# Kernel tuning notes

Hardware: AMD Instinct MI355X
Metric: run time of the kernel (lower is better)

## Reference

```python
import jax, jax.numpy as jnp
import numpy as np

S, B, E, H, V, O = 1024, 256, 128, 256, 32000, 2


def setup_inputs() -> dict:
    key = jax.random.key(0)
    ks = jax.random.split(key, 6)
    inp = jax.random.randint(ks[0], (S, B), 0, V)                     # [S, B] time-major token ids
    lengths = jax.random.randint(ks[1], (B,), 1, S + 1)               # valid lengths in [1, S]
    emb_table = jax.random.normal(ks[2], (V, E), jnp.float32) * 0.1   # nn.Embedding weight
    w_ih = jax.random.normal(ks[3], (4 * H, E), jnp.float32) * 0.05   # LSTM weight_ih_l0 (gate order i,f,g,o)
    w_hh = jax.random.normal(ks[4], (4 * H, H), jnp.float32) * 0.05   # LSTM weight_hh_l0
    b_ih = jnp.zeros((4 * H,), jnp.float32)
    b_hh = jnp.zeros((4 * H,), jnp.float32)
    dec_w = jax.random.normal(ks[5], (O, H), jnp.float32) * 0.05      # decoder Linear (bias=False)
    h0 = jnp.zeros((1, B, H), jnp.float32)
    c0 = jnp.zeros((1, B, H), jnp.float32)
    return dict(inp=inp, lengths=lengths, h0=h0, c0=c0, emb_table=emb_table,
                w_ih=w_ih, w_hh=w_hh, b_ih=b_ih, b_hh=b_hh, dec_w=dec_w)


def reference(inp, lengths, h0, c0, emb_table, w_ih, w_hh, b_ih, b_hh, dec_w):
    emb = emb_table[inp]  # [S, B, E]
    bias = b_ih + b_hh

    def step(carry, x_t):
        h, c = carry
        gates = x_t @ w_ih.T + h @ w_hh.T + bias          # [B, 4H]
        i, f, g, o = jnp.split(gates, 4, axis=-1)         # pytorch gate order i,f,g,o
        i, f, o = jax.nn.sigmoid(i), jax.nn.sigmoid(f), jax.nn.sigmoid(o)
        g = jnp.tanh(g)
        c = f * c + i * g
        h = o * jnp.tanh(c)
        return (h, c), (h, c)

    _, (hs, cs) = jax.lax.scan(step, (h0[0], c0[0]), emb)  # hs, cs: [S, B, H]
    idx = lengths - 1
    b_arange = jnp.arange(B)
    last_h = hs[idx, b_arange]                             # [B, H] output at last valid step
    last_c = cs[idx, b_arange]
    decoded = jax.nn.sigmoid(last_h @ dec_w.T)             # [B, O]
    # packed-RNN final hidden = state at each sequence's own last valid step
    return decoded, (last_h[None], last_c[None])
```

## Files before the change

kernel.cpp:

```cpp
#include <hip/hip_runtime.h>
#include <hip/hip_bf16.h>
#include <hip/hip_fp16.h>

#define S_LEN 1024
#define BATCH 256
#define EDIM  128
#define HDIM  256
#define ODIM  2

typedef unsigned int uint32;
typedef unsigned long long uint64;
typedef _Float16 half_t;
typedef half_t half2v __attribute__((ext_vector_type(2)));
typedef half_t half8  __attribute__((ext_vector_type(8)));
typedef float  f32x4  __attribute__((ext_vector_type(4)));

#define OFF_WHHF   0
#define OFF_WIHF   131072
#define OFF_HBUF   196608
#define HBUF_DW    131072

__device__ __forceinline__ float sigf(float x)     { return 1.0f / (1.0f + __expf(-x)); }
__device__ __forceinline__ float tanhfast(float x) { return 1.0f - 2.0f / (__expf(2.0f * x) + 1.0f); }

__device__ __forceinline__ uint32 packh2(float a, float b) {
  union { uint32 u; half2v h; } c; c.h[0] = (half_t)a; c.h[1] = (half_t)b; return c.u;
}
__device__ __forceinline__ half8 as_h8(uint4 v) {
  union { uint4 u; half8 h; } c; c.u = v; return c.h;
}

__global__ void prep_kernel(const float* __restrict__ w_ih, const float* __restrict__ w_hh,
                            uint32* __restrict__ ws_u) {
  int id = blockIdx.x * 256 + threadIdx.x;
  if (id < 131072) {
    int q = id >> 15, T = (id >> 11) & 15, t = (id >> 8) & 7, l = (id >> 2) & 63, d = id & 3;
    int grow = (T >> 2) * 256 + q * 64 + (T & 3) * 16 + (l & 15);
    int k = t * 32 + (l >> 4) * 8 + 2 * d;
    ws_u[OFF_WHHF + id] = packh2(w_hh[grow * HDIM + k], w_hh[grow * HDIM + k + 1]);
  } else if (id < 131072 + 65536) {
    int i2 = id - 131072;
    int q = i2 >> 14, T = (i2 >> 10) & 15, t = (i2 >> 8) & 3, l = (i2 >> 2) & 63, d = i2 & 3;
    int grow = (T >> 2) * 256 + q * 64 + (T & 3) * 16 + (l & 15);
    int k = t * 32 + (l >> 4) * 8 + 2 * d;
    ws_u[OFF_WIHF + i2] = packh2(w_ih[grow * EDIM + k], w_ih[grow * EDIM + k + 1]);
  } else if (id < 131072 + 65536 + HBUF_DW) {
    ws_u[OFF_HBUF + (id - 131072 - 65536)] = 0;
  }
}

__global__ __launch_bounds__(256, 1) void lstm_kernel(
    const int* __restrict__ inp, const int* __restrict__ lengths,
    const float* __restrict__ h0, const float* __restrict__ c0,
    const float* __restrict__ emb,
    const float* __restrict__ b_ih, const float* __restrict__ b_hh,
    uint32* __restrict__ ws_u,
    float* __restrict__ outh, float* __restrict__ outc) {
  __shared__ uint32 x_l[2 * 16 * 68];
  __shared__ uint32 h_l[16 * 132];
  __shared__ int fast_sh;

  const int tid  = threadIdx.x;
  const int lane = tid & 63, w = tid >> 6;
  const int c = blockIdx.x & 15, q = blockIdx.x >> 4;
  const int n = lane & 15, p = lane >> 4;
  const int sb = tid >> 4, j = tid & 15;

  uint64* hb = (uint64*)(ws_u + OFF_HBUF);

  {
    uint32 xcc;
    asm volatile("s_getreg_b32 %0, hwreg(HW_REG_XCC_ID)" : "=s"(xcc));
    if (tid == 0) {
      int* sl = (int*)(ws_u + OFF_HBUF);
      const int sbase = (16 + c) * 4096;
      __hip_atomic_store(sl + sbase + 64 * q, (int)xcc + 1,
                         __ATOMIC_RELAXED, __HIP_MEMORY_SCOPE_AGENT);
      int ok = 1;
      for (int qq = 0; qq < 4; ++qq) {
        if (qq == q) continue;
        int v;
        do {
          v = __hip_atomic_load(sl + sbase + 64 * qq,
                                __ATOMIC_RELAXED, __HIP_MEMORY_SCOPE_AGENT);
        } while (v == 0);
        ok &= (v == (int)xcc + 1);
      }
      fast_sh = ok;
    }
  }

  int perm[8];
  perm[0] = 2 * q; perm[1] = 2 * q + 1;
#pragma unroll
  for (int i = 2; i < 8; ++i) {
    int base = i - 2;
    perm[i] = base < 2 * q ? base : base + 2;
  }
  int haddr[8];
#pragma unroll
  for (int i = 0; i < 8; ++i) haddr[i] = n * 132 + perm[i] * 16 + p * 4;

  uint4 ahh[4][8], aih[4][4];
  {
    const uint4* whhf = (const uint4*)(ws_u + OFF_WHHF);
    const uint4* wihf = (const uint4*)(ws_u + OFF_WIHF);
#pragma unroll
    for (int g = 0; g < 4; ++g) {
      const int T = g * 4 + w;
#pragma unroll
      for (int i = 0; i < 8; ++i)
        ahh[g][i] = whhf[((q * 16 + T) * 8 + perm[i]) * 64 + lane];
#pragma unroll
      for (int t = 0; t < 4; ++t)
        aih[g][t] = wihf[((q * 16 + T) * 4 + t) * 64 + lane];
    }
  }

  const int ub  = 16 * w + 4 * p;
  const int col = 16 * c + n;
  const int len = lengths[col] - 1;
  float bias_[4][4], cst[4];
#pragma unroll
  for (int g = 0; g < 4; ++g) {
    float4 bi = *(const float4*)(b_ih + g * 256 + q * 64 + ub);
    float4 bh = *(const float4*)(b_hh + g * 256 + q * 64 + ub);
    bias_[g][0] = bi.x + bh.x; bias_[g][1] = bi.y + bh.y;
    bias_[g][2] = bi.z + bh.z; bias_[g][3] = bi.w + bh.w;
  }
  {
    float4 cv = *(const float4*)(c0 + col * HDIM + q * 64 + ub);
    cst[0] = cv.x; cst[1] = cv.y; cst[2] = cv.z; cst[3] = cv.w;
  }

  {
    const float4* hsrc = (const float4*)(h0 + (16 * c + sb) * HDIM) + 4 * j;
    float4 a0 = hsrc[0], a1 = hsrc[1], a2 = hsrc[2], a3 = hsrc[3];
    uint4 pk0 = { packh2(a0.x,a0.y), packh2(a0.z,a0.w), packh2(a1.x,a1.y), packh2(a1.z,a1.w) };
    uint4 pk1 = { packh2(a2.x,a2.y), packh2(a2.z,a2.w), packh2(a3.x,a3.y), packh2(a3.z,a3.w) };
    *(uint4*)(h_l + sb * 132 + 8 * j)     = pk0;
    *(uint4*)(h_l + sb * 132 + 8 * j + 4) = pk1;
    int tok = inp[16 * c + sb];
    const float4* xsrc = (const float4*)(emb + tok * EDIM) + 2 * j;
    float4 v0 = xsrc[0], v1 = xsrc[1];
    uint4 px = { packh2(v0.x,v0.y), packh2(v0.z,v0.w), packh2(v1.x,v1.y), packh2(v1.z,v1.w) };
    *(uint4*)(x_l + sb * 68 + 4 * j) = px;
  }
  __syncthreads();
  const bool fast = (fast_sh != 0);

  int ch[6];
#pragma unroll
  for (int i = 0; i < 6; ++i) {
    int idx6 = j * 6 + i;
    ch[i] = idx6 < q * 32 ? idx6 : idx6 + 32;
  }

  for (int s = 0; s < S_LEN; ++s) {
    const int par = s & 1;

    uint64 hv6[6] = {0, 0, 0, 0, 0, 0};
    const uint64* rp = hb + (((par ^ 1) * 16 + c) * 16 + sb) * 128;
    const uint64 *r0 = rp + ch[0], *r1 = rp + ch[1], *r2 = rp + ch[2],
                 *r3 = rp + ch[3], *r4 = rp + ch[4], *r5 = rp + ch[5];
    if (s > 0) {
      hv6[0] = __hip_atomic_load(r0, __ATOMIC_RELAXED, __HIP_MEMORY_SCOPE_AGENT);
      hv6[1] = __hip_atomic_load(r1, __ATOMIC_RELAXED, __HIP_MEMORY_SCOPE_AGENT);
      hv6[2] = __hip_atomic_load(r2, __ATOMIC_RELAXED, __HIP_MEMORY_SCOPE_AGENT);
      hv6[3] = __hip_atomic_load(r3, __ATOMIC_RELAXED, __HIP_MEMORY_SCOPE_AGENT);
      hv6[4] = __hip_atomic_load(r4, __ATOMIC_RELAXED, __HIP_MEMORY_SCOPE_AGENT);
      hv6[5] = __hip_atomic_load(r5, __ATOMIC_RELAXED, __HIP_MEMORY_SCOPE_AGENT);
    }

    f32x4 acc[4];
#pragma unroll
    for (int g = 0; g < 4; ++g)
      acc[g] = (f32x4){ bias_[g][0], bias_[g][1], bias_[g][2], bias_[g][3] };
#pragma unroll
    for (int t = 0; t < 4; ++t) {
      uint4 xb = *(const uint4*)(x_l + par * 1088 + n * 68 + t * 16 + p * 4);
#pragma unroll
      for (int g = 0; g < 4; ++g)
        acc[g] = __builtin_amdgcn_mfma_f32_16x16x32_f16(as_h8(aih[g][t]), as_h8(xb), acc[g], 0, 0, 0);
    }
#pragma unroll
    for (int i = 0; i < 2; ++i) {
      uint4 hbv = *(const uint4*)(h_l + haddr[i]);
#pragma unroll
      for (int g = 0; g < 4; ++g)
        acc[g] = __builtin_amdgcn_mfma_f32_16x16x32_f16(as_h8(ahh[g][i]), as_h8(hbv), acc[g], 0, 0, 0);
    }

    if (s > 0) {
      const uint32 us = (uint32)s;
      while (!(((uint32)(hv6[0] >> 32) >= us) & ((uint32)(hv6[1] >> 32) >= us) &
               ((uint32)(hv6[2] >> 32) >= us) & ((uint32)(hv6[3] >> 32) >= us) &
               ((uint32)(hv6[4] >> 32) >= us) & ((uint32)(hv6[5] >> 32) >= us))) {
        hv6[0] = __hip_atomic_load(r0, __ATOMIC_RELAXED, __HIP_MEMORY_SCOPE_AGENT);
        hv6[1] = __hip_atomic_load(r1, __ATOMIC_RELAXED, __HIP_MEMORY_SCOPE_AGENT);
        hv6[2] = __hip_atomic_load(r2, __ATOMIC_RELAXED, __HIP_MEMORY_SCOPE_AGENT);
        hv6[3] = __hip_atomic_load(r3, __ATOMIC_RELAXED, __HIP_MEMORY_SCOPE_AGENT);
        hv6[4] = __hip_atomic_load(r4, __ATOMIC_RELAXED, __HIP_MEMORY_SCOPE_AGENT);
        hv6[5] = __hip_atomic_load(r5, __ATOMIC_RELAXED, __HIP_MEMORY_SCOPE_AGENT);
      }
#pragma unroll
      for (int i = 0; i < 6; ++i) h_l[sb * 132 + ch[i]] = (uint32)hv6[i];
    }
    __syncthreads();

    float4 xv0 = {0.f,0.f,0.f,0.f}, xv1 = {0.f,0.f,0.f,0.f};
    if (s + 1 < S_LEN) {
      int tok = inp[(s + 1) * BATCH + 16 * c + sb];
      const float4* xsrc = (const float4*)(emb + tok * EDIM) + 2 * j;
      xv0 = xsrc[0]; xv1 = xsrc[1];
    }

#pragma unroll
    for (int i = 2; i < 8; ++i) {
      uint4 hbv = *(const uint4*)(h_l + haddr[i]);
#pragma unroll
      for (int g = 0; g < 4; ++g)
        acc[g] = __builtin_amdgcn_mfma_f32_16x16x32_f16(as_h8(ahh[g][i]), as_h8(hbv), acc[g], 0, 0, 0);
    }

    float hv4[4];
#pragma unroll
    for (int r = 0; r < 4; ++r) {
      float iv = sigf(acc[0][r]), fv = sigf(acc[1][r]);
      float gv = tanhfast(acc[2][r]), ov = sigf(acc[3][r]);
      float cn = fv * cst[r] + iv * gv;
      cst[r] = cn;
      hv4[r] = ov * tanhfast(cn);
    }

    if (s + 1 < S_LEN) {
      uint32 pay0 = packh2(hv4[0], hv4[1]), pay1 = packh2(hv4[2], hv4[3]);
      const uint32 su = (uint32)(s + 1);
      const int P = q * 32 + 8 * w + 2 * p;
      uint64* wp = hb + (((par * 16 + c) * 16 + n) * 128 + P);
      uint64 pv0 = (uint64)pay0 | (((uint64)su) << 32);
      uint64 pv1 = (uint64)pay1 | (((uint64)su) << 32);
      if (fast) {
        __hip_atomic_store(wp,     pv0, __ATOMIC_RELAXED, __HIP_MEMORY_SCOPE_WORKGROUP);
        __hip_atomic_store(wp + 1, pv1, __ATOMIC_RELAXED, __HIP_MEMORY_SCOPE_WORKGROUP);
      } else {
        __hip_atomic_store(wp,     pv0, __ATOMIC_RELAXED, __HIP_MEMORY_SCOPE_AGENT);
        __hip_atomic_store(wp + 1, pv1, __ATOMIC_RELAXED, __HIP_MEMORY_SCOPE_AGENT);
      }
      *(uint2*)(h_l + n * 132 + P) = (uint2){ pay0, pay1 };
      uint4 px = { packh2(xv0.x,xv0.y), packh2(xv0.z,xv0.w), packh2(xv1.x,xv1.y), packh2(xv1.z,xv1.w) };
      *(uint4*)(x_l + (par ^ 1) * 1088 + sb * 68 + 4 * j) = px;
    }
    if (s == len) {
      float4 ho = { hv4[0], hv4[1], hv4[2], hv4[3] };
      float4 co = { cst[0], cst[1], cst[2], cst[3] };
      *(float4*)(outh + col * HDIM + q * 64 + ub) = ho;
      *(float4*)(outc + col * HDIM + q * 64 + ub) = co;
    }
    __syncthreads();
  }
}

__global__ __launch_bounds__(64) void decode_kernel(const float* __restrict__ outh,
                                                    const float* __restrict__ dec_w,
                                                    float* __restrict__ dec) {
  int b = blockIdx.x, l = threadIdx.x;
  float p0 = 0.f, p1 = 0.f;
#pragma unroll
  for (int m = 0; m < HDIM / 64; ++m) {
    float h = outh[b * HDIM + l + 64 * m];
    p0 = fmaf(h, dec_w[l + 64 * m], p0);
    p1 = fmaf(h, dec_w[HDIM + l + 64 * m], p1);
  }
#pragma unroll
  for (int off = 32; off > 0; off >>= 1) {
    p0 += __shfl_down(p0, off);
    p1 += __shfl_down(p1, off);
  }
  if (l == 0) {
    dec[b * ODIM + 0] = sigf(p0);
    dec[b * ODIM + 1] = sigf(p1);
  }
}

extern "C" void kernel_launch(void* const* d_in, const int* in_sizes, int n_in,
                              void* d_out, int out_size, void* d_ws, size_t ws_size,
                              hipStream_t stream) {
  const int*   inp     = (const int*)d_in[0];
  const int*   lengths = (const int*)d_in[1];
  const float* h0      = (const float*)d_in[2];
  const float* c0      = (const float*)d_in[3];
  const float* emb     = (const float*)d_in[4];
  const float* w_ih    = (const float*)d_in[5];
  const float* w_hh    = (const float*)d_in[6];
  const float* b_ih    = (const float*)d_in[7];
  const float* b_hh    = (const float*)d_in[8];
  const float* dec_w   = (const float*)d_in[9];

  uint32* ws_u = (uint32*)d_ws;

  float* dec  = (float*)d_out;
  float* outh = dec + BATCH * ODIM;
  float* outc = outh + BATCH * HDIM;

  const int prep_total = 131072 + 65536 + HBUF_DW;
  prep_kernel<<<(prep_total + 255) / 256, 256, 0, stream>>>(w_ih, w_hh, ws_u);
  lstm_kernel<<<64, 256, 0, stream>>>(inp, lengths, h0, c0, emb, b_ih, b_hh,
                                      ws_u, outh, outc);
  decode_kernel<<<BATCH, 64, 0, stream>>>(outh, dec_w, dec);
}
```

Before: 2.414 ms.

## Feed remote hidden-state loads directly into MFMA registers, drop mid-step barrier

Each lane now polls exactly the remote h fragments it needs for its own MFMA B operand (permuted chunk offsets) and builds the operand in registers, instead of cooperatively copying into LDS and syncing. This removes one __syncthreads per timestep and the LDS round trip, and prefetches the next token id early. The step barrier is replaced by a manual lgkmcnt wait plus s_barrier with sched barriers. It risks more global polling traffic (24 atomic loads per lane instead of 6) and relies on the perm mapping being correct.

```diff
diff --git a/kernel.cpp b/kernel.cpp
--- a/kernel.cpp
+++ b/kernel.cpp
@@ -149,115 +149,127 @@
   __syncthreads();
   const bool fast = (fast_sh != 0);
 
-  int ch[6];
-#pragma unroll
-  for (int i = 0; i < 6; ++i) {
-    int idx6 = j * 6 + i;
-    ch[i] = idx6 < q * 32 ? idx6 : idx6 + 32;
-  }
-
-  for (int s = 0; s < S_LEN; ++s) {
-    const int par = s & 1;
-
-    uint64 hv6[6] = {0, 0, 0, 0, 0, 0};
-    const uint64* rp = hb + (((par ^ 1) * 16 + c) * 16 + sb) * 128;
-    const uint64 *r0 = rp + ch[0], *r1 = rp + ch[1], *r2 = rp + ch[2],
-                 *r3 = rp + ch[3], *r4 = rp + ch[4], *r5 = rp + ch[5];
-    if (s > 0) {
-      hv6[0] = __hip_atomic_load(r0, __ATOMIC_RELAXED, __HIP_MEMORY_SCOPE_AGENT);
-      hv6[1] = __hip_atomic_load(r1, __ATOMIC_RELAXED, __HIP_MEMORY_SCOPE_AGENT);
-      hv6[2] = __hip_atomic_load(r2, __ATOMIC_RELAXED, __HIP_MEMORY_SCOPE_AGENT);
-      hv6[3] = __hip_atomic_load(r3, __ATOMIC_RELAXED, __HIP_MEMORY_SCOPE_AGENT);
-      hv6[4] = __hip_atomic_load(r4, __ATOMIC_RELAXED, __HIP_MEMORY_SCOPE_AGENT);
-      hv6[5] = __hip_atomic_load(r5, __ATOMIC_RELAXED, __HIP_MEMORY_SCOPE_AGENT);
-    }
-
+  const int p4 = p * 4;
+  const int pbA = perm[2] * 16 + p4, pbB = perm[3] * 16 + p4, pbC = perm[4] * 16 + p4;
+  const int pbD = perm[5] * 16 + p4, pbE = perm[6] * 16 + p4, pbF = perm[7] * 16 + p4;
+
+#define AL(ptr) __hip_atomic_load((ptr), __ATOMIC_RELAXED, __HIP_MEMORY_SCOPE_AGENT)
+#define XMF(t) { uint4 xb = *(const uint4*)(x_l + par * 1088 + n * 68 + (t) * 16 + p4); \
+    acc[0] = __builtin_amdgcn_mfma_f32_16x16x32_f16(as_h8(aih[0][t]), as_h8(xb), acc[0], 0, 0, 0); \
+    acc[1] = __builtin_amdgcn_mfma_f32_16x16x32_f16(as_h8(aih[1][t]), as_h8(xb), acc[1], 0, 0, 0); \
+    acc[2] = __builtin_amdgcn_mfma_f32_16x16x32_f16(as_h8(aih[2][t]), as_h8(xb), acc[2], 0, 0, 0); \
+    acc[3] = __builtin_amdgcn_mfma_f32_16x16x32_f16(as_h8(aih[3][t]), as_h8(xb), acc[3], 0, 0, 0); }
+#define HMF(i) { uint4 hbv = *(const uint4*)(h_l + haddr[i]); \
+    acc[0] = __builtin_amdgcn_mfma_f32_16x16x32_f16(as_h8(ahh[0][i]), as_h8(hbv), acc[0], 0, 0, 0); \
+    acc[1] = __builtin_amdgcn_mfma_f32_16x16x32_f16(as_h8(ahh[1][i]), as_h8(hbv), acc[1], 0, 0, 0); \
+    acc[2] = __builtin_amdgcn_mfma_f32_16x16x32_f16(as_h8(ahh[2][i]), as_h8(hbv), acc[2], 0, 0, 0); \
+    acc[3] = __builtin_amdgcn_mfma_f32_16x16x32_f16(as_h8(ahh[3][i]), as_h8(hbv), acc[3], 0, 0, 0); }
+#define HMFR(L, i) { uint4 hbv = { (uint32)h##L##0, (uint32)h##L##1, (uint32)h##L##2, (uint32)h##L##3 }; \
+    acc[0] = __builtin_amdgcn_mfma_f32_16x16x32_f16(as_h8(ahh[0][i]), as_h8(hbv), acc[0], 0, 0, 0); \
+    acc[1] = __builtin_amdgcn_mfma_f32_16x16x32_f16(as_h8(ahh[1][i]), as_h8(hbv), acc[1], 0, 0, 0); \
+    acc[2] = __builtin_amdgcn_mfma_f32_16x16x32_f16(as_h8(ahh[2][i]), as_h8(hbv), acc[2], 0, 0, 0); \
+    acc[3] = __builtin_amdgcn_mfma_f32_16x16x32_f16(as_h8(ahh[3][i]), as_h8(hbv), acc[3], 0, 0, 0); }
+#define GATES_PUBLISH(sv)                                                                 \
+    float hv4[4];                                                                         \
+    _Pragma("unroll")                                                                     \
+    for (int r = 0; r < 4; ++r) {                                                         \
+      float iv = sigf(acc[0][r]), fv = sigf(acc[1][r]);                                   \
+      float gv = tanhfast(acc[2][r]), ov = sigf(acc[3][r]);                               \
+      float cn = fv * cst[r] + iv * gv;                                                   \
+      cst[r] = cn;                                                                        \
+      hv4[r] = ov * tanhfast(cn);                                                         \
+    }                                                                                     \
+    if ((sv) + 1 < S_LEN) {                                                               \
+      uint32 pay0 = packh2(hv4[0], hv4[1]), pay1 = packh2(hv4[2], hv4[3]);                \
+      const uint32 su = (uint32)((sv) + 1);                                               \
+      const int P = q * 32 + 8 * w + 2 * p;                                               \
+      uint64* wp = hb + ((((sv & 1) * 16 + c) * 16 + n) * 128 + P);                       \
+      uint64 pv0 = (uint64)pay0 | (((uint64)su) << 32);                                   \
+      uint64 pv1 = (uint64)pay1 | (((uint64)su) << 32);                                   \
+      if (fast) {                                                                         \
+        __hip_atomic_store(wp,     pv0, __ATOMIC_RELAXED, __HIP_MEMORY_SCOPE_WORKGROUP);  \
+        __hip_atomic_store(wp + 1, pv1, __ATOMIC_RELAXED, __HIP_MEMORY_SCOPE_WORKGROUP);  \
+      } else {                                                                            \
+        __hip_atomic_store(wp,     pv0, __ATOMIC_RELAXED, __HIP_MEMORY_SCOPE_AGENT);      \
+        __hip_atomic_store(wp + 1, pv1, __ATOMIC_RELAXED, __HIP_MEMORY_SCOPE_AGENT);      \
+      }                                                                                   \
+      *(uint2*)(h_l + n * 132 + P) = (uint2){ pay0, pay1 };                               \
+      uint4 px = { packh2(xv0.x,xv0.y), packh2(xv0.z,xv0.w),                              \
+                   packh2(xv1.x,xv1.y), packh2(xv1.z,xv1.w) };                            \
+      *(uint4*)(x_l + (((sv) & 1) ^ 1) * 1088 + sb * 68 + 4 * j) = px;                    \
+    }                                                                                     \
+    if ((sv) == len) {                                                                    \
+      float4 ho = { hv4[0], hv4[1], hv4[2], hv4[3] };                                     \
+      float4 co = { cst[0], cst[1], cst[2], cst[3] };                                     \
+      *(float4*)(outh + col * HDIM + q * 64 + ub) = ho;                                   \
+      *(float4*)(outc + col * HDIM + q * 64 + ub) = co;                                   \
+    }
+#define STEP_BARRIER do {                                              \
+    asm volatile("s_waitcnt lgkmcnt(0)" ::: "memory");                 \
+    __builtin_amdgcn_sched_barrier(0);                                 \
+    __builtin_amdgcn_s_barrier();                                      \
+    __builtin_amdgcn_sched_barrier(0);                                 \
+  } while (0)
+
+  {
+    const int par = 0;
+    int tok_next = inp[1 * BATCH + 16 * c + sb];
     f32x4 acc[4];
 #pragma unroll
     for (int g = 0; g < 4; ++g)
       acc[g] = (f32x4){ bias_[g][0], bias_[g][1], bias_[g][2], bias_[g][3] };
-#pragma unroll
-    for (int t = 0; t < 4; ++t) {
-      uint4 xb = *(const uint4*)(x_l + par * 1088 + n * 68 + t * 16 + p * 4);
-#pragma unroll
-      for (int g = 0; g < 4; ++g)
-        acc[g] = __builtin_amdgcn_mfma_f32_16x16x32_f16(as_h8(aih[g][t]), as_h8(xb), acc[g], 0, 0, 0);
-    }
-#pragma unroll
-    for (int i = 0; i < 2; ++i) {
-      uint4 hbv = *(const uint4*)(h_l + haddr[i]);
-#pragma unroll
-      for (int g = 0; g < 4; ++g)
-        acc[g] = __builtin_amdgcn_mfma_f32_16x16x32_f16(as_h8(ahh[g][i]), as_h8(hbv), acc[g], 0, 0, 0);
-    }
-
-    if (s > 0) {
+    XMF(0) XMF(1) XMF(2) XMF(3)
+    HMF(0) HMF(1) HMF(2) HMF(3) HMF(4) HMF(5) HMF(6) HMF(7)
+    float4 xv0, xv1;
+    {
+      const float4* xsrc = (const float4*)(emb + tok_next * EDIM) + 2 * j;
+      xv0 = xsrc[0]; xv1 = xsrc[1];
+    }
+    GATES_PUBLISH(0)
+    STEP_BARRIER;
+  }
+
+  for (int s = 1; s < S_LEN; ++s) {
+    const int par = s & 1;
+    const uint64* rp = hb + (((par ^ 1) * 16 + c) * 16 + n) * 128;
+
+    uint64 hA0, hA1, hA2, hA3, hB0, hB1, hB2, hB3, hC0, hC1, hC2, hC3;
+    uint64 hD0, hD1, hD2, hD3, hE0, hE1, hE2, hE3, hF0, hF1, hF2, hF3;
+#define ISS(L, pb) h##L##0 = AL(rp + (pb) + 0); h##L##1 = AL(rp + (pb) + 1); \
+                   h##L##2 = AL(rp + (pb) + 2); h##L##3 = AL(rp + (pb) + 3);
+    ISS(A, pbA) ISS(B, pbB) ISS(C, pbC) ISS(D, pbD) ISS(E, pbE) ISS(F, pbF)
+    int tok_next = 0;
+    if (s + 1 < S_LEN) tok_next = inp[(s + 1) * BATCH + 16 * c + sb];
+
+    f32x4 acc[4];
+#pragma unroll
+    for (int g = 0; g < 4; ++g)
+      acc[g] = (f32x4){ bias_[g][0], bias_[g][1], bias_[g][2], bias_[g][3] };
+    XMF(0) XMF(1) XMF(2) XMF(3)
+    HMF(0) HMF(1)
+
+    {
       const uint32 us = (uint32)s;
-      while (!(((uint32)(hv6[0] >> 32) >= us) & ((uint32)(hv6[1] >> 32) >= us) &
-               ((uint32)(hv6[2] >> 32) >= us) & ((uint32)(hv6[3] >> 32) >= us) &
-               ((uint32)(hv6[4] >> 32) >= us) & ((uint32)(hv6[5] >> 32) >= us))) {
-        hv6[0] = __hip_atomic_load(r0, __ATOMIC_RELAXED, __HIP_MEMORY_SCOPE_AGENT);
-        hv6[1] = __hip_atomic_load(r1, __ATOMIC_RELAXED, __HIP_MEMORY_SCOPE_AGENT);
-        hv6[2] = __hip_atomic_load(r2, __ATOMIC_RELAXED, __HIP_MEMORY_SCOPE_AGENT);
-        hv6[3] = __hip_atomic_load(r3, __ATOMIC_RELAXED, __HIP_MEMORY_SCOPE_AGENT);
-        hv6[4] = __hip_atomic_load(r4, __ATOMIC_RELAXED, __HIP_MEMORY_SCOPE_AGENT);
-        hv6[5] = __hip_atomic_load(r5, __ATOMIC_RELAXED, __HIP_MEMORY_SCOPE_AGENT);
+#define CHK6(L) (((uint32)(h##L##0 >> 32) < us) | ((uint32)(h##L##1 >> 32) < us) | \
+                 ((uint32)(h##L##2 >> 32) < us) | ((uint32)(h##L##3 >> 32) < us))
+      while (true) {
+        uint32 bad = CHK6(A) | CHK6(B) | CHK6(C) | CHK6(D) | CHK6(E) | CHK6(F);
+        if (!bad) break;
+        ISS(A, pbA) ISS(B, pbB) ISS(C, pbC) ISS(D, pbD) ISS(E, pbE) ISS(F, pbF)
       }
-#pragma unroll
-      for (int i = 0; i < 6; ++i) h_l[sb * 132 + ch[i]] = (uint32)hv6[i];
-    }
-    __syncthreads();
+#undef CHK6
+    }
 
     float4 xv0 = {0.f,0.f,0.f,0.f}, xv1 = {0.f,0.f,0.f,0.f};
     if (s + 1 < S_LEN) {
-      int tok = inp[(s + 1) * BATCH + 16 * c + sb];
-      const float4* xsrc = (const float4*)(emb + tok * EDIM) + 2 * j;
+      const float4* xsrc = (const float4*)(emb + tok_next * EDIM) + 2 * j;
       xv0 = xsrc[0]; xv1 = xsrc[1];
     }
 
-#pragma unroll
-    for (int i = 2; i < 8; ++i) {
-      uint4 hbv = *(const uint4*)(h_l + haddr[i]);
-#pragma unroll
-      for (int g = 0; g < 4; ++g)
-        acc[g] = __builtin_amdgcn_mfma_f32_16x16x32_f16(as_h8(ahh[g][i]), as_h8(hbv), acc[g], 0, 0, 0);
-    }
-
-    float hv4[4];
-#pragma unroll
-    for (int r = 0; r < 4; ++r) {
-      float iv = sigf(acc[0][r]), fv = sigf(acc[1][r]);
-      float gv = tanhfast(acc[2][r]), ov = sigf(acc[3][r]);
-      float cn = fv * cst[r] + iv * gv;
-      cst[r] = cn;
-      hv4[r] = ov * tanhfast(cn);
-    }
-
-    if (s + 1 < S_LEN) {
-      uint32 pay0 = packh2(hv4[0], hv4[1]), pay1 = packh2(hv4[2], hv4[3]);
-      const uint32 su = (uint32)(s + 1);
-      const int P = q * 32 + 8 * w + 2 * p;
-      uint64* wp = hb + (((par * 16 + c) * 16 + n) * 128 + P);
-      uint64 pv0 = (uint64)pay0 | (((uint64)su) << 32);
-      uint64 pv1 = (uint64)pay1 | (((uint64)su) << 32);
-      if (fast) {
-        __hip_atomic_store(wp,     pv0, __ATOMIC_RELAXED, __HIP_MEMORY_SCOPE_WORKGROUP);
-        __hip_atomic_store(wp + 1, pv1, __ATOMIC_RELAXED, __HIP_MEMORY_SCOPE_WORKGROUP);
-      } else {
-        __hip_atomic_store(wp,     pv0, __ATOMIC_RELAXED, __HIP_MEMORY_SCOPE_AGENT);
-        __hip_atomic_store(wp + 1, pv1, __ATOMIC_RELAXED, __HIP_MEMORY_SCOPE_AGENT);
-      }
-      *(uint2*)(h_l + n * 132 + P) = (uint2){ pay0, pay1 };
-      uint4 px = { packh2(xv0.x,xv0.y), packh2(xv0.z,xv0.w), packh2(xv1.x,xv1.y), packh2(xv1.z,xv1.w) };
-      *(uint4*)(x_l + (par ^ 1) * 1088 + sb * 68 + 4 * j) = px;
-    }
-    if (s == len) {
-      float4 ho = { hv4[0], hv4[1], hv4[2], hv4[3] };
-      float4 co = { cst[0], cst[1], cst[2], cst[3] };
-      *(float4*)(outh + col * HDIM + q * 64 + ub) = ho;
-      *(float4*)(outc + col * HDIM + q * 64 + ub) = co;
-    }
-    __syncthreads();
+    HMFR(A, 2) HMFR(B, 3) HMFR(C, 4) HMFR(D, 5) HMFR(E, 6) HMFR(F, 7)
+
+    GATES_PUBLISH(s)
+    STEP_BARRIER;
   }
 }
 
```

After: 5.175 ms. 2.14x slower.
